# Performance work log

Hardware: AMD Instinct MI355X
Metric: run time of the kernel (lower is better)

## Reference

```python
import jax, jax.numpy as jnp
import numpy as np

NUM_EXPERTS = 8
TOP_K = 2
HIDDEN = 2048
FFN = 4096


def setup_inputs() -> dict:
    key = jax.random.key(0)
    ks = jax.random.split(key, 5)
    s = 0.02
    return {
        "hidden_states": jax.random.normal(ks[0], (2, 2048, HIDDEN), dtype=jnp.float32),
        "w_router": jax.random.normal(ks[1], (HIDDEN, NUM_EXPERTS), dtype=jnp.float32) * s,
        "w1": jax.random.normal(ks[2], (NUM_EXPERTS, FFN, HIDDEN), dtype=jnp.float32) * s,
        "w2": jax.random.normal(ks[3], (NUM_EXPERTS, HIDDEN, FFN), dtype=jnp.float32) * s,
        "w3": jax.random.normal(ks[4], (NUM_EXPERTS, FFN, HIDDEN), dtype=jnp.float32) * s,
    }


def reference(hidden_states, w_router, w1, w2, w3):
    shape = hidden_states.shape
    x = hidden_states.reshape(-1, HIDDEN)  # [T, H]

    # Router: logits -> softmax -> top-k -> renormalize (Mixtral routing)
    logits = x @ w_router                              # [T, E]
    probs = jax.nn.softmax(logits, axis=-1)
    top_w, top_i = jax.lax.top_k(probs, TOP_K)         # [T, K]
    top_w = top_w / jnp.sum(top_w, axis=-1, keepdims=True)
    # Dense combine weights per expert: [T, E]
    combine = jnp.sum(
        jax.nn.one_hot(top_i, NUM_EXPERTS, dtype=x.dtype) * top_w[..., None], axis=1
    )

    # Grouped SwiGLU experts: out = sum_e combine[:, e] * w2_e(silu(w1_e x) * w3_e x)
    out = jnp.zeros_like(x)
    for e in range(NUM_EXPERTS):
        h = jax.nn.silu(x @ w1[e].T) * (x @ w3[e].T)   # [T, F]
        y = h @ w2[e].T                                # [T, H]
        out = out + combine[:, e:e + 1] * y

    return (out.reshape(shape), jnp.zeros((1,), dtype=x.dtype))
```

## Files before the change

kernel.cpp:

```cpp
#include <hip/hip_runtime.h>
#include <hip/hip_bf16.h>
#include <stdint.h>

#define T_TOK 4096
#define HID   2048
#define FFN_D 4096
#define NE    8
#define PADB  256

typedef __attribute__((ext_vector_type(8))) short  short8;
typedef __attribute__((ext_vector_type(4))) float  f32x4;
typedef __attribute__((ext_vector_type(4))) unsigned short u16x4;
typedef unsigned short u16;

__device__ __forceinline__ u16 f2bf(float f) {
    unsigned u = __float_as_uint(f);
    u += 0x7FFFu + ((u >> 16) & 1u);
    return (u16)(u >> 16);
}
__device__ __forceinline__ float bf2f(u16 v) {
    return __uint_as_float(((unsigned)v) << 16);
}

#define GLD16(g, l) __builtin_amdgcn_global_load_lds( \
    (const __attribute__((address_space(1))) unsigned int*)(g), \
    (__attribute__((address_space(3))) unsigned int*)(l), 16, 0, 0)

__global__ void k_convert(const float* __restrict__ s, u16* __restrict__ d, long n8) {
    for (long i = (long)blockIdx.x * 256 + threadIdx.x; i < n8; i += (long)gridDim.x * 256) {
        f32x4 a = *((const f32x4*)s + i * 2);
        f32x4 b = *((const f32x4*)s + i * 2 + 1);
        short8 o;
#pragma unroll
        for (int q = 0; q < 4; ++q) { o[q] = (short)f2bf(a[q]); o[q + 4] = (short)f2bf(b[q]); }
        *(short8*)(d + i * 8) = o;
    }
}

__global__ void k_router(const float* __restrict__ x, const float* __restrict__ wr,
                         int* __restrict__ topk_id, float* __restrict__ topk_w,
                         int* __restrict__ counts) {
    int lane = threadIdx.x & 63;
    int t = blockIdx.x * 4 + (threadIdx.x >> 6);
    const float* xr = x + (size_t)t * HID;
    float acc[8];
#pragma unroll
    for (int e = 0; e < 8; ++e) acc[e] = 0.f;
    for (int h = lane; h < HID; h += 64) {
        float xv = xr[h];
        f32x4 w0 = *(const f32x4*)(wr + h * 8);
        f32x4 w1 = *(const f32x4*)(wr + h * 8 + 4);
#pragma unroll
        for (int q = 0; q < 4; ++q) { acc[q] += xv * w0[q]; acc[4 + q] += xv * w1[q]; }
    }
#pragma unroll
    for (int e = 0; e < 8; ++e) {
        float v = acc[e];
#pragma unroll
        for (int s = 32; s > 0; s >>= 1) v += __shfl_xor(v, s);
        acc[e] = v;
    }
    if (lane == 0) {
        int i0 = 0; float l0 = acc[0];
#pragma unroll
        for (int e = 1; e < 8; ++e) if (acc[e] > l0) { l0 = acc[e]; i0 = e; }
        int i1 = -1; float l1 = -3.4e38f;
#pragma unroll
        for (int e = 0; e < 8; ++e) if (e != i0 && acc[e] > l1) { l1 = acc[e]; i1 = e; }
        float wA = 1.f / (1.f + expf(l1 - l0));
        topk_id[t * 2] = i0;  topk_id[t * 2 + 1] = i1;
        topk_w[t * 2] = wA;   topk_w[t * 2 + 1] = 1.f - wA;
        atomicAdd(&counts[i0], 1);
        atomicAdd(&counts[i1], 1);
    }
}

__global__ void k_scan(const int* __restrict__ counts, int* __restrict__ pad_off,
                       int* __restrict__ perm_tok) {
    __shared__ int sTot;
    if (threadIdx.x == 0) {
        int o = 0;
#pragma unroll
        for (int e = 0; e < 8; ++e) { pad_off[e] = o; o += ((counts[e] + PADB - 1) / PADB) * PADB; }
        pad_off[8] = o; sTot = o;
    }
    __syncthreads();
    int tot = sTot;
    for (int i = threadIdx.x; i < tot; i += 256) perm_tok[i] = 0;
}

__global__ void k_scatter(const int* __restrict__ topk_id, int* __restrict__ cursors,
                          const int* __restrict__ pad_off, int* __restrict__ perm_tok,
                          int* __restrict__ pos_of) {
    int t = blockIdx.x * 256 + threadIdx.x;
    if (t >= T_TOK) return;
#pragma unroll
    for (int k = 0; k < 2; ++k) {
        int e = topk_id[t * 2 + k];
        int p = pad_off[e] + atomicAdd(&cursors[e], 1);
        perm_tok[p] = t;
        pos_of[t * 2 + k] = p;
    }
}

template<int KTOT, int NTOT, int BNt, bool DUAL, bool GATHER>
__global__ __launch_bounds__(512, 2) void k_gemm8(
    const u16* __restrict__ A,
    const u16* __restrict__ B0all,
    const u16* __restrict__ B1all,
    u16* __restrict__ C,
    const int* __restrict__ perm_tok,
    const int* __restrict__ pad_off)
{
    constexpr int BMt   = 256;
    constexpr int WCW   = BNt / 4;
    constexpr int NI    = WCW / 16;
    constexpr int CPX   = (NTOT / BNt) / 8;
    constexpr int NK    = KTOT / 64;
    constexpr int ATILE = BMt * 64;
    constexpr int BTILE = BNt * 64;
    constexpr int SEGB  = DUAL ? 8 : (BNt == 256 ? 8 : 4);

    const int bid = blockIdx.x;
    const int xcd = bid & 7;
    const int idx = bid >> 3;
    const int m0  = (idx / CPX) * BMt;
    if (m0 >= pad_off[8]) return;
    const int n0  = (xcd * CPX + (idx % CPX)) * BNt;
    int e = 0;
    while (pad_off[e + 1] <= m0) ++e;

    __shared__ u16 As[2 * ATILE];
    __shared__ u16 Bs0[2 * BTILE];
    __shared__ u16 Bs1[DUAL ? 2 * BTILE : 8];
    __shared__ int tokS[GATHER ? BMt : 8];

    const int tid = threadIdx.x;
    const int w = tid >> 6, l = tid & 63;
    if (GATHER) {
        for (int i = tid; i < BMt; i += 512) tokS[i] = perm_tok[m0 + i];
        __syncthreads();
    }

    const u16* B0 = B0all + (size_t)e * NTOT * KTOT;
    const u16* B1 = DUAL ? (B1all + (size_t)e * NTOT * KTOT) : B0all;

    const int nseg = (w < 4) ? 8 : SEGB;
    const u16* gsrc[8];
    u16* ldst[8];
    int tstep;
    {
        const int c = (l & 7) ^ (l >> 3);
#pragma unroll
        for (int j = 0; j < 8; ++j) {
            const int js = (j < nseg) ? j : (j - 4);
            const int rl = js * 8 + (l >> 3);
            if (w < 4) {
                const int rt = w * 64 + rl;
                const long grow = GATHER ? (long)tokS[rt] : (long)(m0 + rt);
                gsrc[j] = A + grow * KTOT + c * 8;
                ldst[j] = (u16*)As + (w * 64 + js * 8) * 64;
                tstep = ATILE;
            } else if (DUAL && w >= 6) {
                const int rt = (w - 6) * 64 + rl;
                gsrc[j] = B1 + (size_t)(n0 + rt) * KTOT + c * 8;
                ldst[j] = (u16*)Bs1 + (rt - rl + js * 8) * 64;
                tstep = BTILE;
            } else {
                const int rt = DUAL ? ((w - 4) * 64 + rl)
                                    : (BNt == 256 ? ((w - 4) * 64 + rl)
                                                  : ((w - 4) * 32 + rl));
                gsrc[j] = B0 + (size_t)(n0 + rt) * KTOT + c * 8;
                ldst[j] = (u16*)Bs0 + (rt - rl + js * 8) * 64;
                tstep = BTILE;
            }
        }
    }

    const int wr = w >> 2, wc = w & 3;
    const int fr = l & 15, fk = l >> 4, x7 = l & 7;
    const int pc0 = ((fk ^ x7) << 3);
    const int pc1 = pc0 ^ 32;
    const int aB = (wr * 128 + fr) * 64;
    const int bB = (wc * WCW + fr) * 64;

    f32x4 acc0[8][NI], acc1[8][NI];
    const f32x4 fz = {0.f, 0.f, 0.f, 0.f};
#pragma unroll
    for (int mi = 0; mi < 8; ++mi)
#pragma unroll
        for (int ni = 0; ni < NI; ++ni) { acc0[mi][ni] = fz; if (DUAL) acc1[mi][ni] = fz; }

#pragma unroll
    for (int j = 0; j < 8; ++j) if (j < nseg) GLD16(gsrc[j], ldst[j]);
    asm volatile("s_waitcnt vmcnt(0)" ::: "memory");
    __builtin_amdgcn_s_barrier();
    __builtin_amdgcn_sched_barrier(0);

#pragma unroll 1
    for (int t = 0; t < NK; ++t) {
        const int cb = t & 1, nb2 = cb ^ 1;
        const u16* aC  = (const u16*)As  + cb * ATILE;
        const u16* b0C = (const u16*)Bs0 + cb * BTILE;
        const u16* b1C = (const u16*)Bs1 + (DUAL ? cb * BTILE : 0);
        const long kE = (long)(t + 1) * 64;
        const bool hasNext = (t + 1 < NK);

        short8 af[4], b0f[NI], b1f[NI];

        if (hasNext) {
#pragma unroll
            for (int j = 0; j < 4; ++j) if (j < nseg) GLD16(gsrc[j] + kE, ldst[j] + nb2 * tstep);
        }
#pragma unroll
        for (int mi = 0; mi < 4; ++mi) af[mi] = *(const short8*)(aC + aB + mi * 1024 + pc0);
#pragma unroll
        for (int ni = 0; ni < NI; ++ni) {
            b0f[ni] = *(const short8*)(b0C + bB + ni * 1024 + pc0);
            if (DUAL) b1f[ni] = *(const short8*)(b1C + bB + ni * 1024 + pc0);
        }
        __builtin_amdgcn_s_setprio(1);
#pragma unroll
        for (int mi = 0; mi < 4; ++mi)
#pragma unroll
            for (int ni = 0; ni < NI; ++ni) {
                acc0[mi][ni] = __builtin_amdgcn_mfma_f32_16x16x32_bf16(af[mi], b0f[ni], acc0[mi][ni], 0, 0, 0);
                if (DUAL)
                    acc1[mi][ni] = __builtin_amdgcn_mfma_f32_16x16x32_bf16(af[mi], b1f[ni], acc1[mi][ni], 0, 0, 0);
            }
        __builtin_amdgcn_s_setprio(0);

        if (hasNext) {
#pragma unroll
            for (int j = 4; j < 8; ++j) if (j < nseg) GLD16(gsrc[j] + kE, ldst[j] + nb2 * tstep);
        }
#pragma unroll
        for (int mi = 0; mi < 4; ++mi) af[mi] = *(const short8*)(aC + aB + (mi + 4) * 1024 + pc0);
        __builtin_amdgcn_s_setprio(1);
#pragma unroll
        for (int mi = 0; mi < 4; ++mi)
#pragma unroll
            for (int ni = 0; ni < NI; ++ni) {
                acc0[mi + 4][ni] = __builtin_amdgcn_mfma_f32_16x16x32_bf16(af[mi], b0f[ni], acc0[mi + 4][ni], 0, 0, 0);
                if (DUAL)
                    acc1[mi + 4][ni] = __builtin_amdgcn_mfma_f32_16x16x32_bf16(af[mi], b1f[ni], acc1[mi + 4][ni], 0, 0, 0);
            }
        __builtin_amdgcn_s_setprio(0);

#pragma unroll
        for (int mi = 0; mi < 4; ++mi) af[mi] = *(const short8*)(aC + aB + mi * 1024 + pc1);
#pragma unroll
        for (int ni = 0; ni < NI; ++ni) {
            b0f[ni] = *(const short8*)(b0C + bB + ni * 1024 + pc1);
            if (DUAL) b1f[ni] = *(const short8*)(b1C + bB + ni * 1024 + pc1);
        }
        __builtin_amdgcn_s_setprio(1);
#pragma unroll
        for (int mi = 0; mi < 4; ++mi)
#pragma unroll
            for (int ni = 0; ni < NI; ++ni) {
                acc0[mi][ni] = __builtin_amdgcn_mfma_f32_16x16x32_bf16(af[mi], b0f[ni], acc0[mi][ni], 0, 0, 0);
                if (DUAL)
                    acc1[mi][ni] = __builtin_amdgcn_mfma_f32_16x16x32_bf16(af[mi], b1f[ni], acc1[mi][ni], 0, 0, 0);
            }
        __builtin_amdgcn_s_setprio(0);

#pragma unroll
        for (int mi = 0; mi < 4; ++mi) af[mi] = *(const short8*)(aC + aB + (mi + 4) * 1024 + pc1);
        __builtin_amdgcn_s_setprio(1);
#pragma unroll
        for (int mi = 0; mi < 4; ++mi)
#pragma unroll
            for (int ni = 0; ni < NI; ++ni) {
                acc0[mi + 4][ni] = __builtin_amdgcn_mfma_f32_16x16x32_bf16(af[mi], b0f[ni], acc0[mi + 4][ni], 0, 0, 0);
                if (DUAL)
                    acc1[mi + 4][ni] = __builtin_amdgcn_mfma_f32_16x16x32_bf16(af[mi], b1f[ni], acc1[mi + 4][ni], 0, 0, 0);
            }
        __builtin_amdgcn_s_setprio(0);

        asm volatile("s_waitcnt vmcnt(0)" ::: "memory");
        __builtin_amdgcn_s_barrier();
        __builtin_amdgcn_sched_barrier(0);
    }

    const int er = (l >> 4) * 4;
    const int ec = l & 15;
#pragma unroll
    for (int mi = 0; mi < 8; ++mi)
#pragma unroll
        for (int ni = 0; ni < NI; ++ni)
#pragma unroll
            for (int r = 0; r < 4; ++r) {
                size_t prow = (size_t)(m0 + wr * 128 + mi * 16 + er + r);
                int col = n0 + wc * WCW + ni * 16 + ec;
                float v = acc0[mi][ni][r];
                float res;
                if (DUAL) {
                    float g3 = acc1[mi][ni][r];
                    res = v / (1.f + __expf(-v)) * g3;
                } else {
                    res = v;
                }
                C[prow * NTOT + col] = f2bf(res);
            }
}

__global__ void k_combine(const u16* __restrict__ y, const int* __restrict__ pos_of,
                          const float* __restrict__ topk_w, float* __restrict__ out) {
    int idx = blockIdx.x * 256 + threadIdx.x;
    int t  = idx >> 9;
    int c4 = (idx & 511) << 2;
    int p0 = pos_of[t * 2], p1 = pos_of[t * 2 + 1];
    float w0 = topk_w[t * 2], w1 = topk_w[t * 2 + 1];
    u16x4 a = *(const u16x4*)(y + (size_t)p0 * HID + c4);
    u16x4 b = *(const u16x4*)(y + (size_t)p1 * HID + c4);
    f32x4 o;
#pragma unroll
    for (int q = 0; q < 4; ++q) o[q] = w0 * bf2f(a[q]) + w1 * bf2f(b[q]);
    *(f32x4*)(out + (size_t)t * HID + c4) = o;
    if (idx == 0) out[(size_t)T_TOK * HID] = 0.f;
}

__global__ void k_init(int* __restrict__ c) {
    if (threadIdx.x < 16) c[threadIdx.x] = 0;
}

extern "C" void kernel_launch(void* const* d_in, const int* in_sizes, int n_in,
                              void* d_out, int out_size, void* d_ws, size_t ws_size,
                              hipStream_t stream) {
    const float* x  = (const float*)d_in[0];
    const float* wr = (const float*)d_in[1];
    const float* w1 = (const float*)d_in[2];
    const float* w2 = (const float*)d_in[3];
    const float* w3 = (const float*)d_in[4];
    float* out = (float*)d_out;
    char* ws = (char*)d_ws;

    u16*  xb  = (u16*)(ws);
    u16*  wA  = (u16*)(ws + 16777216);
    u16*  w3b = (u16*)(ws + 150994944);
    u16*  hb  = (u16*)(ws + 285212672);
    u16*  yb  = (u16*)(ws + 150994944);
    int*  perm_tok = (int*)(ws + 369098752);
    int*  pos_of   = (int*)(ws + 369139712);
    int*  topk_id  = (int*)(ws + 369172480);
    float* topk_w  = (float*)(ws + 369205248);
    int*  cnt      = (int*)(ws + 369238016);
    int*  counts   = cnt;
    int*  cursors  = cnt + 8;
    int*  pad_off  = cnt + 16;

    k_init<<<1, 64, 0, stream>>>(cnt);
    k_convert<<<2048, 256, 0, stream>>>(x, xb, (long)T_TOK * HID / 8);
    k_router<<<1024, 256, 0, stream>>>(x, wr, topk_id, topk_w, counts);
    k_scan<<<1, 256, 0, stream>>>(counts, pad_off, perm_tok);
    k_scatter<<<16, 256, 0, stream>>>(topk_id, cursors, pad_off, perm_tok, pos_of);

    const long WN8 = (long)NE * FFN_D * HID / 8;
    k_convert<<<4096, 256, 0, stream>>>(w1, wA, WN8);
    k_convert<<<4096, 256, 0, stream>>>(w3, w3b, WN8);

    k_gemm8<HID, FFN_D, 128, true, true><<<(FFN_D / 128) * 40, 512, 0, stream>>>(
        xb, wA, w3b, hb, perm_tok, pad_off);

    k_convert<<<4096, 256, 0, stream>>>(w2, wA, WN8);

    k_gemm8<FFN_D, HID, 128, false, false><<<(HID / 128) * 40, 512, 0, stream>>>(
        hb, wA, (const u16*)nullptr, yb, perm_tok, pad_off);

    k_combine<<<8192, 256, 0, stream>>>(yb, pos_of, topk_w, out);
}
```

Measured before the change: 946.5 us.

## Split-K the down-projection GEMM with wider N tiles and sum partials in combine

```diff
diff --git a/kernel.cpp b/kernel.cpp
--- a/kernel.cpp
+++ b/kernel.cpp
@@ -7,6 +7,7 @@
 #define FFN_D 4096
 #define NE    8
 #define PADB  256
+#define PADMAX 10240
 
 typedef __attribute__((ext_vector_type(8))) short  short8;
 typedef __attribute__((ext_vector_type(4))) float  f32x4;
@@ -103,7 +104,7 @@
     }
 }
 
-template<int KTOT, int NTOT, int BNt, bool DUAL, bool GATHER>
+template<int KTOT, int NTOT, int BNt, int KSPLIT, bool DUAL, bool GATHER>
 __global__ __launch_bounds__(512, 2) void k_gemm8(
     const u16* __restrict__ A,
     const u16* __restrict__ B0all,
@@ -116,14 +117,17 @@
     constexpr int WCW   = BNt / 4;
     constexpr int NI    = WCW / 16;
     constexpr int CPX   = (NTOT / BNt) / 8;
-    constexpr int NK    = KTOT / 64;
+    constexpr int KPART = KTOT / KSPLIT;
+    constexpr int NK    = KPART / 64;
     constexpr int ATILE = BMt * 64;
     constexpr int BTILE = BNt * 64;
     constexpr int SEGB  = DUAL ? 8 : (BNt == 256 ? 8 : 4);
 
     const int bid = blockIdx.x;
     const int xcd = bid & 7;
-    const int idx = bid >> 3;
+    int idx = bid >> 3;
+    const int kh  = idx & (KSPLIT - 1);
+    idx /= KSPLIT;
     const int m0  = (idx / CPX) * BMt;
     if (m0 >= pad_off[8]) return;
     const int n0  = (xcd * CPX + (idx % CPX)) * BNt;
@@ -144,6 +148,7 @@
 
     const u16* B0 = B0all + (size_t)e * NTOT * KTOT;
     const u16* B1 = DUAL ? (B1all + (size_t)e * NTOT * KTOT) : B0all;
+    const int k0e = kh * KPART;
 
     const int nseg = (w < 4) ? 8 : SEGB;
     const u16* gsrc[8];
@@ -158,19 +163,19 @@
             if (w < 4) {
                 const int rt = w * 64 + rl;
                 const long grow = GATHER ? (long)tokS[rt] : (long)(m0 + rt);
-                gsrc[j] = A + grow * KTOT + c * 8;
+                gsrc[j] = A + grow * KTOT + k0e + c * 8;
                 ldst[j] = (u16*)As + (w * 64 + js * 8) * 64;
                 tstep = ATILE;
             } else if (DUAL && w >= 6) {
                 const int rt = (w - 6) * 64 + rl;
-                gsrc[j] = B1 + (size_t)(n0 + rt) * KTOT + c * 8;
+                gsrc[j] = B1 + (size_t)(n0 + rt) * KTOT + k0e + c * 8;
                 ldst[j] = (u16*)Bs1 + (rt - rl + js * 8) * 64;
                 tstep = BTILE;
             } else {
                 const int rt = DUAL ? ((w - 4) * 64 + rl)
                                     : (BNt == 256 ? ((w - 4) * 64 + rl)
                                                   : ((w - 4) * 32 + rl));
-                gsrc[j] = B0 + (size_t)(n0 + rt) * KTOT + c * 8;
+                gsrc[j] = B0 + (size_t)(n0 + rt) * KTOT + k0e + c * 8;
                 ldst[j] = (u16*)Bs0 + (rt - rl + js * 8) * 64;
                 tstep = BTILE;
             }
@@ -283,6 +288,7 @@
         __builtin_amdgcn_sched_barrier(0);
     }
 
+    u16* Co = C + (KSPLIT > 1 ? (size_t)kh * PADMAX * NTOT : 0);
     const int er = (l >> 4) * 4;
     const int ec = l & 15;
 #pragma unroll
@@ -301,22 +307,26 @@
                 } else {
                     res = v;
                 }
-                C[prow * NTOT + col] = f2bf(res);
-            }
-}
-
-__global__ void k_combine(const u16* __restrict__ y, const int* __restrict__ pos_of,
-                          const float* __restrict__ topk_w, float* __restrict__ out) {
+                Co[prow * NTOT + col] = f2bf(res);
+            }
+}
+
+__global__ void k_combine2(const u16* __restrict__ y0, const u16* __restrict__ y1,
+                           const int* __restrict__ pos_of,
+                           const float* __restrict__ topk_w, float* __restrict__ out) {
     int idx = blockIdx.x * 256 + threadIdx.x;
     int t  = idx >> 9;
     int c4 = (idx & 511) << 2;
     int p0 = pos_of[t * 2], p1 = pos_of[t * 2 + 1];
     float w0 = topk_w[t * 2], w1 = topk_w[t * 2 + 1];
-    u16x4 a = *(const u16x4*)(y + (size_t)p0 * HID + c4);
-    u16x4 b = *(const u16x4*)(y + (size_t)p1 * HID + c4);
+    u16x4 a0 = *(const u16x4*)(y0 + (size_t)p0 * HID + c4);
+    u16x4 a1 = *(const u16x4*)(y1 + (size_t)p0 * HID + c4);
+    u16x4 b0 = *(const u16x4*)(y0 + (size_t)p1 * HID + c4);
+    u16x4 b1 = *(const u16x4*)(y1 + (size_t)p1 * HID + c4);
     f32x4 o;
 #pragma unroll
-    for (int q = 0; q < 4; ++q) o[q] = w0 * bf2f(a[q]) + w1 * bf2f(b[q]);
+    for (int q = 0; q < 4; ++q)
+        o[q] = w0 * (bf2f(a0[q]) + bf2f(a1[q])) + w1 * (bf2f(b0[q]) + bf2f(b1[q]));
     *(f32x4*)(out + (size_t)t * HID + c4) = o;
     if (idx == 0) out[(size_t)T_TOK * HID] = 0.f;
 }
@@ -360,13 +370,14 @@
     k_convert<<<4096, 256, 0, stream>>>(w1, wA, WN8);
     k_convert<<<4096, 256, 0, stream>>>(w3, w3b, WN8);
 
-    k_gemm8<HID, FFN_D, 128, true, true><<<(FFN_D / 128) * 40, 512, 0, stream>>>(
+    k_gemm8<HID, FFN_D, 128, 1, true, true><<<(FFN_D / 128) * 40, 512, 0, stream>>>(
         xb, wA, w3b, hb, perm_tok, pad_off);
 
     k_convert<<<4096, 256, 0, stream>>>(w2, wA, WN8);
 
-    k_gemm8<FFN_D, HID, 128, false, false><<<(HID / 128) * 40, 512, 0, stream>>>(
+    k_gemm8<FFN_D, HID, 256, 2, false, false><<<(HID / 256) * 40 * 2, 512, 0, stream>>>(
         hb, wA, (const u16*)nullptr, yb, perm_tok, pad_off);
 
-    k_combine<<<8192, 256, 0, stream>>>(yb, pos_of, topk_w, out);
-}
+    k_combine2<<<8192, 256, 0, stream>>>(yb, yb + (size_t)PADMAX * HID,
+                                         pos_of, topk_w, out);
+}
```

Result: faster. 869.8 us (-8.1%).
